# Kernel optimization log

Measured on AMD Instinct MI355X. Metric: run time of the kernel, lower is better.

Reference implementation:

```python
import jax, jax.numpy as jnp
import numpy as np

N = 50000
E = 800000
D_IN = 384
D_H = 128
D_MLP = 128
K = 16


def layer_norm(x, g, b, eps=1e-5):
    m = x.mean(-1, keepdims=True)
    v = ((x - m) ** 2).mean(-1, keepdims=True)
    return (x - m) / jnp.sqrt(v + eps) * g + b


def setup_inputs() -> dict:
    key = jax.random.key(0)
    ks = jax.random.split(key, 16)
    s = lambda d: 1.0 / np.sqrt(d)
    return {
        "x": jax.random.normal(ks[0], (N, D_IN), jnp.float32),
        "edge_index": jax.random.randint(ks[1], (2, E), 0, N, jnp.int64),
        # GCNConv 1
        "W1": jax.random.normal(ks[2], (D_IN, D_H), jnp.float32) * s(D_IN),
        "b1": jnp.zeros((D_H,), jnp.float32),
        "g1": jnp.ones((D_H,), jnp.float32),
        "be1": jnp.zeros((D_H,), jnp.float32),
        # GCNConv 2
        "W2": jax.random.normal(ks[3], (D_H, D_H), jnp.float32) * s(D_H),
        "b2": jnp.zeros((D_H,), jnp.float32),
        "g2": jnp.ones((D_H,), jnp.float32),
        "be2": jnp.zeros((D_H,), jnp.float32),
        # residual projection (input_dim != conv_hidden)
        "rW": jax.random.normal(ks[4], (D_IN, D_H), jnp.float32) * s(D_IN),
        "rb": jnp.zeros((D_H,), jnp.float32),
        "rg": jnp.ones((D_H,), jnp.float32),
        "rbe": jnp.zeros((D_H,), jnp.float32),
        # MLP head
        "mW1": jax.random.normal(ks[5], (D_H, D_MLP), jnp.float32) * s(D_H),
        "mb1": jnp.zeros((D_MLP,), jnp.float32),
        "mg": jnp.ones((D_MLP,), jnp.float32),
        "mbe": jnp.zeros((D_MLP,), jnp.float32),
        "mW2": jax.random.normal(ks[6], (D_MLP, K), jnp.float32) * s(D_MLP),
        "mb2": jnp.zeros((K,), jnp.float32),
    }


def reference(x, edge_index, W1, b1, g1, be1, W2, b2, g2, be2,
              rW, rb, rg, rbe, mW1, mb1, mg, mbe, mW2, mb2):
    n = x.shape[0]
    loops = jnp.arange(n, dtype=edge_index.dtype)
    src = jnp.concatenate([edge_index[0], loops])  # [E+N]
    dst = jnp.concatenate([edge_index[1], loops])
    # symmetric GCN normalization with self-loops
    deg = jax.ops.segment_sum(jnp.ones_like(src, x.dtype), dst, num_segments=n)
    dinv = jnp.where(deg > 0, jax.lax.rsqrt(deg), 0.0)
    norm = dinv[src] * dinv[dst]  # [E+N]

    def gcn_conv(h, W, b):
        hw = h @ W  # [N, D_H]
        msg = hw[src] * norm[:, None]  # gather + scale, [E+N, D_H]
        return jax.ops.segment_sum(msg, dst, num_segments=n) + b

    # layer 1 with projected residual
    h = jax.nn.elu(layer_norm(gcn_conv(x, W1, b1), g1, be1))
    h = h + layer_norm(x @ rW + rb, rg, rbe)
    # layer 2 with identity residual
    h = jax.nn.elu(layer_norm(gcn_conv(h, W2, b2), g2, be2)) + h
    # MLP head (dropout inactive in eval) + softmax over clusters
    z = jax.nn.elu(layer_norm(h @ mW1 + mb1, mg, mbe))
    H = z @ mW2 + mb2
    return jax.nn.softmax(H, axis=1)
```

## Files before the change

### kernel.cpp

```cpp
#include <hip/hip_runtime.h>

#define DH 128

typedef __attribute__((ext_vector_type(8))) short short8;
typedef __attribute__((ext_vector_type(4))) float f32x4;

__device__ __forceinline__ float wave_sum(float v) {
    #pragma unroll
    for (int o = 32; o > 0; o >>= 1) v += __shfl_xor(v, o, 64);
    return v;
}

__device__ __forceinline__ void ln_pair(float v0, float v1, float& o0, float& o1) {
    float m = wave_sum(v0 + v1) * (1.f / 128.f);
    float d0 = v0 - m, d1 = v1 - m;
    float var = wave_sum(d0 * d0 + d1 * d1) * (1.f / 128.f);
    float inv = rsqrtf(var + 1e-5f);
    o0 = d0 * inv; o1 = d1 * inv;
}

__device__ __forceinline__ float elu(float x) { return x > 0.f ? x : expm1f(x); }

__device__ __forceinline__ unsigned short f2bf(float f) {
    unsigned u = __float_as_uint(f);
    u += 0x7fffu + ((u >> 16) & 1u);
    return (unsigned short)(u >> 16);
}
__device__ __forceinline__ float bfl(unsigned u) { return __uint_as_float(u << 16); }
__device__ __forceinline__ float bfh(unsigned u) { return __uint_as_float(u & 0xffff0000u); }
__device__ __forceinline__ unsigned pack_bf2(float a, float b) {
    return (unsigned)f2bf(a) | ((unsigned)f2bf(b) << 16);
}
__device__ __forceinline__ short8 cvt8(float4 v0, float4 v1) {
    short8 o;
    o[0] = (short)f2bf(v0.x); o[1] = (short)f2bf(v0.y);
    o[2] = (short)f2bf(v0.z); o[3] = (short)f2bf(v0.w);
    o[4] = (short)f2bf(v1.x); o[5] = (short)f2bf(v1.y);
    o[6] = (short)f2bf(v1.z); o[7] = (short)f2bf(v1.w);
    return o;
}

__device__ __forceinline__ int xcd_work(int bid, int nwg) {
    int qc = nwg >> 3, rc = nwg & 7;
    int xcd = bid & 7, ix = bid >> 3;
    return (xcd < rc ? xcd * (qc + 1) : rc * (qc + 1) + (xcd - rc) * qc) + ix;
}

__global__ void deg_count_k(const int* __restrict__ dst, int* __restrict__ deg, int E) {
    int e = blockIdx.x * 256 + threadIdx.x;
    if (e < E) atomicAdd(&deg[dst[e]], 1);
}

__global__ __launch_bounds__(1024) void scan_part_k(const int* __restrict__ deg,
                                                    int* __restrict__ rowptr,
                                                    int* __restrict__ bsum,
                                                    float* __restrict__ dinv, int n)
{
    __shared__ int wsum[16];
    const int tid = threadIdx.x, lane = tid & 63, wid = tid >> 6;
    int i = blockIdx.x * 1024 + tid;
    int v = (i < n) ? deg[i] : 0;
    if (i < n) dinv[i] = rsqrtf((float)(v + 1));
    int s = v;
    #pragma unroll
    for (int o = 1; o < 64; o <<= 1) {
        int t = __shfl_up(s, o, 64);
        if (lane >= o) s += t;
    }
    if (lane == 63) wsum[wid] = s;
    __syncthreads();
    if (tid < 16) {
        int ws = wsum[tid];
        #pragma unroll
        for (int o = 1; o < 16; o <<= 1) {
            int t = __shfl_up(ws, o, 64);
            if (tid >= o) ws += t;
        }
        wsum[tid] = ws;
    }
    __syncthreads();
    int excl = (wid ? wsum[wid - 1] : 0) + s - v;
    if (i < n) rowptr[i] = excl;
    if (tid == 0) bsum[blockIdx.x] = wsum[15];
}

__global__ void scan_top_k(int* __restrict__ bsum, int* __restrict__ rowptr_n, int nb) {
    int lane = threadIdx.x;
    int carry = 0;
    for (int base = 0; base < nb; base += 64) {
        int i = base + lane;
        int v = (i < nb) ? bsum[i] : 0;
        int s = v;
        #pragma unroll
        for (int o = 1; o < 64; o <<= 1) {
            int t = __shfl_up(s, o, 64);
            if (lane >= o) s += t;
        }
        if (i < nb) bsum[i] = carry + s - v;
        carry += __shfl(s, 63, 64);
    }
    if (lane == 0) *rowptr_n = carry;
}

__global__ void scan_add_k(const int* __restrict__ bsum, int* __restrict__ rowptr,
                           int* __restrict__ cursor, int n)
{
    int i = blockIdx.x * 256 + threadIdx.x;
    if (i < n) {
        int v = rowptr[i] + bsum[i >> 10];
        rowptr[i] = v;
        cursor[i] = v;
    }
}

__global__ void fill_k(const int* __restrict__ src, const int* __restrict__ dst,
                       const float* __restrict__ dinv, int* __restrict__ cursor,
                       int2* __restrict__ csr, int E)
{
    int e = blockIdx.x * 256 + threadIdx.x;
    if (e < E) {
        int s = src[e], d = dst[e];
        float w = dinv[s] * dinv[d];
        int p = atomicAdd(&cursor[d], 1);
        csr[p] = make_int2(s, __float_as_int(w));
    }
}

__global__ void repack_zero_k(const float* __restrict__ W1, const float* __restrict__ rW,
                              const float* __restrict__ W2, const float* __restrict__ mW1,
                              unsigned short* __restrict__ Wp, int* __restrict__ deg, int n)
{
    int idx = blockIdx.x * 256 + threadIdx.x;
    if (idx < n) deg[idx] = 0;
    if (idx >= 131072) return;
    const float* W; int base;
    if (idx < 49152)       { W = W1;  base = 0; }
    else if (idx < 98304)  { W = rW;  base = 49152; }
    else if (idx < 114688) { W = W2;  base = 98304; }
    else                   { W = mW1; base = 114688; }
    int l = idx - base;
    int kb = l >> 12, rem = l & 4095;
    int nn = rem >> 5, ki = rem & 31;
    Wp[idx] = f2bf(W[(kb * 32 + ki) * DH + nn]);
}

__global__ __launch_bounds__(256, 4) void gemm1_k(
    const float* __restrict__ Af,
    const unsigned short* __restrict__ Bp1, const unsigned short* __restrict__ Bp2,
    const float* __restrict__ bb,
    unsigned short* __restrict__ outa, unsigned short* __restrict__ outb, int n)
{
    constexpr int K = 384, NKB = 12;
    __shared__ __align__(16) unsigned short smem[12288];
    unsigned short* smB = smem + 8192;

    const int tid = threadIdx.x;
    const int wid = tid >> 6, lane = tid & 63;
    const int m16 = lane & 15, q = lane >> 4;

    const int work = xcd_work(blockIdx.x, gridDim.x);
    const int rblk = work >> 2;
    const int var  = work & 3;
    const int mat = var >> 1;
    const int c0  = (var & 1) * 64;
    const unsigned short* Bp = mat ? Bp2 : Bp1;
    unsigned short* outp = mat ? outb : outa;
    const float* bias = mat ? bb : nullptr;
    const long long rowbase = (long long)rblk * 128;

    const int row_s0 = tid >> 2, c16_0 = tid & 3;
    const int row_s1 = (tid + 256) >> 2;
    long long gr0 = rowbase + row_s0; if (gr0 > (long long)n - 1) gr0 = n - 1;
    long long gr1 = rowbase + row_s1; if (gr1 > (long long)n - 1) gr1 = n - 1;
    const float* pA0 = Af + gr0 * K + c16_0 * 8;
    const float* pA1 = Af + gr1 * K + c16_0 * 8;
    unsigned short* dA0 = smem + row_s0 * 32 + ((c16_0 ^ (row_s0 & 3)) * 8);
    unsigned short* dA1 = smem + row_s1 * 32 + ((c16_0 ^ (row_s1 & 3)) * 8);
    const unsigned short* pB = Bp + c0 * 32 + tid * 8;
    unsigned short* dB = smB + (tid & 3) * 512 + (tid >> 2) * 8;

    float4 raf[2][2][2];
    short8 rbv[2];

    auto loadT = [&](int kb, int buf) {
        raf[buf][0][0] = *(const float4*)(pA0 + kb * 32);
        raf[buf][0][1] = *(const float4*)(pA0 + kb * 32 + 4);
        raf[buf][1][0] = *(const float4*)(pA1 + kb * 32);
        raf[buf][1][1] = *(const float4*)(pA1 + kb * 32 + 4);
        rbv[buf] = *(const short8*)(pB + kb * 4096);
    };
    auto writeT = [&](int buf) {
        *(short8*)(dA0 + buf * 4096) = cvt8(raf[buf][0][0], raf[buf][0][1]);
        *(short8*)(dA1 + buf * 4096) = cvt8(raf[buf][1][0], raf[buf][1][1]);
        *(short8*)(dB + buf * 2048) = rbv[buf];
    };

    f32x4 acc[2][4];
    const f32x4 zero = {0.f, 0.f, 0.f, 0.f};
    #pragma unroll
    for (int mi = 0; mi < 2; ++mi)
        #pragma unroll
        for (int nj = 0; nj < 4; ++nj) acc[mi][nj] = zero;

    const int frow = wid * 32 + m16;
    const unsigned short* fa_base = smem + frow * 32 + ((q ^ (m16 & 3)) * 8);
    const unsigned short* fb_base = smB + q * 512 + m16 * 8;

    loadT(0, 0);
    loadT(1, 1);
    writeT(0);
    __syncthreads();

    #pragma unroll
    for (int kb = 0; kb < NKB; ++kb) {
        const int buf = kb & 1;
        short8 af0 = *(const short8*)(fa_base + buf * 4096);
        short8 af1 = *(const short8*)(fa_base + buf * 4096 + 512);
        short8 bf[4];
        #pragma unroll
        for (int nj = 0; nj < 4; ++nj)
            bf[nj] = *(const short8*)(fb_base + buf * 2048 + nj * 128);
        if (kb + 2 < NKB) loadT(kb + 2, kb & 1);
        if (kb + 1 < NKB) writeT((kb + 1) & 1);
        #pragma unroll
        for (int nj = 0; nj < 4; ++nj) {
            acc[0][nj] = __builtin_amdgcn_mfma_f32_16x16x32_bf16(af0, bf[nj], acc[0][nj], 0, 0, 0);
            acc[1][nj] = __builtin_amdgcn_mfma_f32_16x16x32_bf16(af1, bf[nj], acc[1][nj], 0, 0, 0);
        }
        __syncthreads();
    }

    #pragma unroll
    for (int nj = 0; nj < 4; ++nj) {
        int cl = nj * 16 + m16;
        float bv = bias ? bias[c0 + cl] : 0.f;
        #pragma unroll
        for (int mi = 0; mi < 2; ++mi)
            #pragma unroll
            for (int r = 0; r < 4; ++r)
                smem[(wid * 32 + mi * 16 + q * 4 + r) * 72 + cl] = f2bf(acc[mi][nj][r] + bv);
    }
    __syncthreads();
    #pragma unroll
    for (int h = 0; h < 4; ++h) {
        int idx = tid + h * 256;
        int row = idx >> 3, c8 = idx & 7;
        long long grow = rowbase + row;
        if (grow < n)
            *(short8*)(outp + grow * DH + c0 + c8 * 8) = *(const short8*)(smem + row * 72 + c8 * 8);
    }
}

__global__ __launch_bounds__(256, 3) void gemm_k128(
    const unsigned short* __restrict__ A,
    const unsigned short* __restrict__ Bp, const float* __restrict__ bias,
    unsigned short* __restrict__ outp, int n)
{
    __shared__ __align__(16) unsigned short smem[24576];
    unsigned short* smB = smem + 16384;

    const int tid = threadIdx.x;
    const int wid = tid >> 6, lane = tid & 63;
    const int m16 = lane & 15, q = lane >> 4;

    const int work = xcd_work(blockIdx.x, gridDim.x);
    const int rblk = work >> 1;
    const int c0 = (work & 1) * 64;
    const long long rowbase = (long long)rblk * 128;

    #pragma unroll
    for (int r = 0; r < 8; ++r) {
        int j = r * 256 + tid;
        int row = j >> 4, c16 = j & 15;
        long long grow = rowbase + row; if (grow > (long long)n - 1) grow = n - 1;
        *(short8*)(smem + row * 128 + ((c16 ^ (row & 15)) * 8)) =
            *(const short8*)(A + grow * 128 + c16 * 8);
    }
    #pragma unroll
    for (int r = 0; r < 4; ++r) {
        int j = r * 256 + tid;
        int kb = j >> 8, rem = j & 255;
        int cl = rem >> 2, qq = rem & 3;
        *(short8*)(smB + kb * 2048 + qq * 512 + cl * 8) =
            *(const short8*)(Bp + kb * 4096 + c0 * 32 + rem * 8);
    }
    __syncthreads();

    f32x4 acc[2][4];
    const f32x4 zero = {0.f, 0.f, 0.f, 0.f};
    #pragma unroll
    for (int mi = 0; mi < 2; ++mi)
        #pragma unroll
        for (int nj = 0; nj < 4; ++nj) acc[mi][nj] = zero;

    const int frow = wid * 32 + m16;
    #pragma unroll
    for (int kb = 0; kb < 4; ++kb) {
        short8 af0 = *(const short8*)(smem + frow * 128 + (((kb * 4 + q) ^ m16) * 8));
        short8 af1 = *(const short8*)(smem + (frow + 16) * 128 + (((kb * 4 + q) ^ m16) * 8));
        #pragma unroll
        for (int nj = 0; nj < 4; ++nj) {
            short8 bf = *(const short8*)(smB + kb * 2048 + q * 512 + (nj * 16 + m16) * 8);
            acc[0][nj] = __builtin_amdgcn_mfma_f32_16x16x32_bf16(af0, bf, acc[0][nj], 0, 0, 0);
            acc[1][nj] = __builtin_amdgcn_mfma_f32_16x16x32_bf16(af1, bf, acc[1][nj], 0, 0, 0);
        }
    }

    __syncthreads();
    #pragma unroll
    for (int nj = 0; nj < 4; ++nj) {
        int cl = nj * 16 + m16;
        float bv = bias ? bias[c0 + cl] : 0.f;
        #pragma unroll
        for (int mi = 0; mi < 2; ++mi)
            #pragma unroll
            for (int r = 0; r < 4; ++r)
                smem[(wid * 32 + mi * 16 + q * 4 + r) * 72 + cl] = f2bf(acc[mi][nj][r] + bv);
    }
    __syncthreads();
    #pragma unroll
    for (int h = 0; h < 4; ++h) {
        int idx = tid + h * 256;
        int row = idx >> 3, c8 = idx & 7;
        long long grow = rowbase + row;
        if (grow < n)
            *(short8*)(outp + grow * DH + c0 + c8 * 8) = *(const short8*)(smem + row * 72 + c8 * 8);
    }
}

__device__ __forceinline__ void gather_row(
    const unsigned* __restrict__ hw, const int2* __restrict__ csr,
    int beg, int end, int lane, float& o0, float& o1)
{
    float a0 = 0.f, a1 = 0.f, b0 = 0.f, b1 = 0.f;
    float c0 = 0.f, c1 = 0.f, d0 = 0.f, d1 = 0.f;
    int p = beg;
    for (; p + 7 < end; p += 8) {
        int2 e0 = csr[p],     e1 = csr[p + 1], e2 = csr[p + 2], e3 = csr[p + 3];
        int2 e4 = csr[p + 4], e5 = csr[p + 5], e6 = csr[p + 6], e7 = csr[p + 7];
        unsigned u0 = hw[(long long)e0.x * 64 + lane];
        unsigned u1 = hw[(long long)e1.x * 64 + lane];
        unsigned u2 = hw[(long long)e2.x * 64 + lane];
        unsigned u3 = hw[(long long)e3.x * 64 + lane];
        unsigned u4 = hw[(long long)e4.x * 64 + lane];
        unsigned u5 = hw[(long long)e5.x * 64 + lane];
        unsigned u6 = hw[(long long)e6.x * 64 + lane];
        unsigned u7 = hw[(long long)e7.x * 64 + lane];
        float w0 = __int_as_float(e0.y), w1 = __int_as_float(e1.y);
        float w2 = __int_as_float(e2.y), w3 = __int_as_float(e3.y);
        float w4 = __int_as_float(e4.y), w5 = __int_as_float(e5.y);
        float w6 = __int_as_float(e6.y), w7 = __int_as_float(e7.y);
        a0 = fmaf(w0, bfl(u0), a0);  a1 = fmaf(w0, bfh(u0), a1);
        b0 = fmaf(w1, bfl(u1), b0);  b1 = fmaf(w1, bfh(u1), b1);
        c0 = fmaf(w2, bfl(u2), c0);  c1 = fmaf(w2, bfh(u2), c1);
        d0 = fmaf(w3, bfl(u3), d0);  d1 = fmaf(w3, bfh(u3), d1);
        a0 = fmaf(w4, bfl(u4), a0);  a1 = fmaf(w4, bfh(u4), a1);
        b0 = fmaf(w5, bfl(u5), b0);  b1 = fmaf(w5, bfh(u5), b1);
        c0 = fmaf(w6, bfl(u6), c0);  c1 = fmaf(w6, bfh(u6), c1);
        d0 = fmaf(w7, bfl(u7), d0);  d1 = fmaf(w7, bfh(u7), d1);
    }
    for (; p + 3 < end; p += 4) {
        int2 e0 = csr[p], e1 = csr[p + 1], e2 = csr[p + 2], e3 = csr[p + 3];
        unsigned u0 = hw[(long long)e0.x * 64 + lane];
        unsigned u1 = hw[(long long)e1.x * 64 + lane];
        unsigned u2 = hw[(long long)e2.x * 64 + lane];
        unsigned u3 = hw[(long long)e3.x * 64 + lane];
        float w0 = __int_as_float(e0.y), w1 = __int_as_float(e1.y);
        float w2 = __int_as_float(e2.y), w3 = __int_as_float(e3.y);
        a0 = fmaf(w0, bfl(u0), a0);  a1 = fmaf(w0, bfh(u0), a1);
        b0 = fmaf(w1, bfl(u1), b0);  b1 = fmaf(w1, bfh(u1), b1);
        c0 = fmaf(w2, bfl(u2), c0);  c1 = fmaf(w2, bfh(u2), c1);
        d0 = fmaf(w3, bfl(u3), d0);  d1 = fmaf(w3, bfh(u3), d1);
    }
    for (; p < end; ++p) {
        int2 e0 = csr[p];
        unsigned u0 = hw[(long long)e0.x * 64 + lane];
        float w0 = __int_as_float(e0.y);
        a0 = fmaf(w0, bfl(u0), a0);
        a1 = fmaf(w0, bfh(u0), a1);
    }
    o0 = (a0 + b0) + (c0 + d0);
    o1 = (a1 + b1) + (c1 + d1);
}

__global__ __launch_bounds__(256) void gfuse1_k(
    const unsigned* __restrict__ hw, const unsigned* __restrict__ proj,
    const int* __restrict__ rowptr, const int2* __restrict__ csr,
    const float* __restrict__ dinv,
    const float* __restrict__ b1, const float* __restrict__ g1, const float* __restrict__ be1,
    const float* __restrict__ rg, const float* __restrict__ rbe,
    unsigned* __restrict__ hout, int n)
{
    int row = blockIdx.x * 4 + (threadIdx.x >> 6);
    if (row >= n) return;
    int lane = threadIdx.x & 63;
    float a0, a1;
    gather_row(hw, csr, rowptr[row], rowptr[row + 1], lane, a0, a1);
    long long off = (long long)row * 64;
    float di = dinv[row], sl = di * di;
    unsigned us = hw[off + lane];
    float2 bv  = *(const float2*)(b1 + 2 * lane);
    float2 gv  = *(const float2*)(g1 + 2 * lane);
    float2 bev = *(const float2*)(be1 + 2 * lane);
    float2 rgv = *(const float2*)(rg + 2 * lane);
    float2 rbv = *(const float2*)(rbe + 2 * lane);
    float v0 = a0 + sl * bfl(us) + bv.x;
    float v1 = a1 + sl * bfh(us) + bv.y;
    float o0, o1; ln_pair(v0, v1, o0, o1);
    float t0 = elu(o0 * gv.x + bev.x);
    float t1 = elu(o1 * gv.y + bev.y);
    unsigned up = proj[off + lane];
    float q0, q1; ln_pair(bfl(up), bfh(up), q0, q1);
    hout[off + lane] = pack_bf2(t0 + q0 * rgv.x + rbv.x, t1 + q1 * rgv.y + rbv.y);
}

__global__ __launch_bounds__(256) void gfuse2_k(
    const unsigned* __restrict__ hw, const unsigned* __restrict__ hprev,
    const int* __restrict__ rowptr, const int2* __restrict__ csr,
    const float* __restrict__ dinv,
    const float* __restrict__ b2, const float* __restrict__ g2, const float* __restrict__ be2,
    unsigned* __restrict__ h2, int n)
{
    int row = blockIdx.x * 4 + (threadIdx.x >> 6);
    if (row >= n) return;
    int lane = threadIdx.x & 63;
    float a0, a1;
    gather_row(hw, csr, rowptr[row], rowptr[row + 1], lane, a0, a1);
    long long off = (long long)row * 64;
    float di = dinv[row], sl = di * di;
    unsigned us = hw[off + lane];
    float2 bv  = *(const float2*)(b2 + 2 * lane);
    float2 gv  = *(const float2*)(g2 + 2 * lane);
    float2 bev = *(const float2*)(be2 + 2 * lane);
    float v0 = a0 + sl * bfl(us) + bv.x;
    float v1 = a1 + sl * bfh(us) + bv.y;
    float o0, o1; ln_pair(v0, v1, o0, o1);
    float t0 = elu(o0 * gv.x + bev.x);
    float t1 = elu(o1 * gv.y + bev.y);
    unsigned uh = hprev[off + lane];
    h2[off + lane] = pack_bf2(t0 + bfl(uh), t1 + bfh(uh));
}

__global__ __launch_bounds__(256) void head_k(
    const unsigned* __restrict__ zraw, const float* __restrict__ g, const float* __restrict__ be,
    const float* __restrict__ mW2, const float* __restrict__ mb2,
    float* __restrict__ out, int n)
{
    int row = blockIdx.x * 4 + (threadIdx.x >> 6);
    if (row >= n) return;
    int lane = threadIdx.x & 63;
    unsigned u = zraw[(long long)row * 64 + lane];
    float o0, o1; ln_pair(bfl(u), bfh(u), o0, o1);
    float2 gv  = *(const float2*)(g + 2 * lane);
    float2 bev = *(const float2*)(be + 2 * lane);
    float z0 = elu(o0 * gv.x + bev.x);
    float z1 = elu(o1 * gv.y + bev.y);
    int k = lane & 15, seg = lane >> 4;
    float acc = 0.f;
    #pragma unroll
    for (int t = 0; t < 16; ++t) {
        int srcl = seg * 16 + t;
        float zz0 = __shfl(z0, srcl, 64);
        float zz1 = __shfl(z1, srcl, 64);
        int c = seg * 32 + 2 * t;
        acc = fmaf(zz0, mW2[c * 16 + k], acc);
        acc = fmaf(zz1, mW2[(c + 1) * 16 + k], acc);
    }
    acc += __shfl_xor(acc, 32, 64);
    acc += __shfl_xor(acc, 16, 64);
    float hk = acc + mb2[k];
    float mx = hk;
    #pragma unroll
    for (int o = 8; o > 0; o >>= 1) mx = fmaxf(mx, __shfl_xor(mx, o, 64));
    float e = expf(hk - mx);
    float s = e;
    #pragma unroll
    for (int o = 8; o > 0; o >>= 1) s += __shfl_xor(s, o, 64);
    if (lane < 16) out[(long long)row * 16 + k] = e / s;
}

static inline size_t align16(size_t x) { return (x + 15) & ~(size_t)15; }

extern "C" void kernel_launch(void* const* d_in, const int* in_sizes, int n_in,
                              void* d_out, int out_size, void* d_ws, size_t ws_size,
                              hipStream_t stream)
{
    const float* x   = (const float*)d_in[0];
    const int*   ei  = (const int*)d_in[1];
    const float* W1  = (const float*)d_in[2];
    const float* b1  = (const float*)d_in[3];
    const float* g1  = (const float*)d_in[4];
    const float* be1 = (const float*)d_in[5];
    const float* W2  = (const float*)d_in[6];
    const float* b2  = (const float*)d_in[7];
    const float* g2  = (const float*)d_in[8];
    const float* be2 = (const float*)d_in[9];
    const float* rW  = (const float*)d_in[10];
    const float* rb  = (const float*)d_in[11];
    const float* rg  = (const float*)d_in[12];
    const float* rbe = (const float*)d_in[13];
    const float* mW1 = (const float*)d_in[14];
    const float* mb1 = (const float*)d_in[15];
    const float* mg  = (const float*)d_in[16];
    const float* mbe = (const float*)d_in[17];
    const float* mW2 = (const float*)d_in[18];
    const float* mb2 = (const float*)d_in[19];
    float* out = (float*)d_out;

    const int n = in_sizes[0] / 384;
    const int E = in_sizes[1] / 2;
    const int* src = ei;
    const int* dst = ei + E;

    char* w = (char*)d_ws;
    int* deg     = (int*)w;   w += align16((size_t)n * 4);
    int* rowptr  = (int*)w;   w += align16((size_t)(n + 1) * 4);
    int* cursor  = (int*)w;   w += align16((size_t)n * 4);
    float* dinv  = (float*)w; w += align16((size_t)n * 4);
    int* bsum    = (int*)w;   w += align16((size_t)1024 * 4);
    int2* csr    = (int2*)w;  w += align16((size_t)E * 8);
    unsigned short* hw1  = (unsigned short*)w; w += align16((size_t)n * DH * 2);
    unsigned short* proj = (unsigned short*)w; w += align16((size_t)n * DH * 2);
    unsigned short* hbuf = (unsigned short*)w; w += align16((size_t)n * DH * 2);
    unsigned short* Wp   = (unsigned short*)w; w += align16((size_t)131072 * 2);
    unsigned short* Wp1 = Wp;
    unsigned short* Wpr = Wp + 49152;
    unsigned short* Wp2 = Wp + 98304;
    unsigned short* WpM = Wp + 114688;
    unsigned short* hw2  = hw1;
    unsigned short* h2   = proj;
    unsigned short* zraw = hbuf;

    int gE = (E + 255) / 256;
    int gN = (n + 255) / 256;
    int nb = (n + 1023) / 1024;
    int rblks = (n + 127) / 128;
    int gRow4 = (n + 3) / 4;

    repack_zero_k<<<512, 256, 0, stream>>>(W1, rW, W2, mW1, Wp, deg, n);

    deg_count_k<<<gE, 256, 0, stream>>>(dst, deg, E);
    scan_part_k<<<nb, 1024, 0, stream>>>(deg, rowptr, bsum, dinv, n);
    scan_top_k<<<1, 64, 0, stream>>>(bsum, rowptr + n, nb);
    scan_add_k<<<gN, 256, 0, stream>>>(bsum, rowptr, cursor, n);
    fill_k<<<gE, 256, 0, stream>>>(src, dst, dinv, cursor, csr, E);

    gemm1_k<<<rblks * 4, 256, 0, stream>>>(x, Wp1, Wpr, rb, hw1, proj, n);
    gfuse1_k<<<gRow4, 256, 0, stream>>>((unsigned*)hw1, (unsigned*)proj, rowptr, csr, dinv,
                                        b1, g1, be1, rg, rbe, (unsigned*)hbuf, n);

    gemm_k128<<<rblks * 2, 256, 0, stream>>>(hbuf, Wp2, nullptr, hw2, n);
    gfuse2_k<<<gRow4, 256, 0, stream>>>((unsigned*)hw2, (unsigned*)hbuf, rowptr, csr, dinv,
                                        b2, g2, be2, (unsigned*)h2, n);

    gemm_k128<<<rblks * 2, 256, 0, stream>>>(h2, WpM, mb1, zraw, n);
    head_k<<<gRow4, 256, 0, stream>>>((unsigned*)zraw, mg, mbe, mW2, mb2, out, n);
}
```

Baseline: 408.6 us.

## Partition CSR fill by XCD destination range and deepen gather unrolling

The CSR fill kernel now assigns each of 8 block groups (blockIdx & 7, matching round-robin XCD dispatch) a contiguous range of destination nodes. Each group scans all edges and only processes those whose destination falls in its range, so cursor atomics and CSR writes for a given node stay within one XCD's L2. The cost is that every group rereads the full dst array. Separately, the gather loop is unrolled to 16 outstanding row loads per iteration, with readfirstlane on the bounds, to raise memory-level parallelism at the cost of more registers.

```diff
diff --git a/kernel.cpp b/kernel.cpp
--- a/kernel.cpp
+++ b/kernel.cpp
@@ -113,16 +113,25 @@
     }
 }
 
-__global__ void fill_k(const int* __restrict__ src, const int* __restrict__ dst,
-                       const float* __restrict__ dinv, int* __restrict__ cursor,
-                       int2* __restrict__ csr, int E)
-{
-    int e = blockIdx.x * 256 + threadIdx.x;
-    if (e < E) {
-        int s = src[e], d = dst[e];
-        float w = dinv[s] * dinv[d];
-        int p = atomicAdd(&cursor[d], 1);
-        csr[p] = make_int2(s, __float_as_int(w));
+__global__ __launch_bounds__(256) void fill_xcd_k(
+    const int* __restrict__ src, const int* __restrict__ dst,
+    const float* __restrict__ dinv, int* __restrict__ cursor,
+    int2* __restrict__ csr, int E, int n)
+{
+    const int g   = blockIdx.x & 7;
+    const int j   = blockIdx.x >> 3;
+    const int bpg = gridDim.x >> 3;
+    const int per = (n + 7) >> 3;
+    const int lo = g * per;
+    const int hi = min(n, lo + per);
+    for (int e = j * 256 + threadIdx.x; e < E; e += bpg * 256) {
+        int d = dst[e];
+        if (d >= lo && d < hi) {
+            int s = src[e];
+            float w = dinv[s] * dinv[d];
+            int p = atomicAdd(&cursor[d], 1);
+            csr[p] = make_int2(s, __float_as_int(w));
+        }
     }
 }
 
@@ -332,32 +341,27 @@
     const unsigned* __restrict__ hw, const int2* __restrict__ csr,
     int beg, int end, int lane, float& o0, float& o1)
 {
+    beg = __builtin_amdgcn_readfirstlane(beg);
+    end = __builtin_amdgcn_readfirstlane(end);
     float a0 = 0.f, a1 = 0.f, b0 = 0.f, b1 = 0.f;
     float c0 = 0.f, c1 = 0.f, d0 = 0.f, d1 = 0.f;
     int p = beg;
-    for (; p + 7 < end; p += 8) {
-        int2 e0 = csr[p],     e1 = csr[p + 1], e2 = csr[p + 2], e3 = csr[p + 3];
-        int2 e4 = csr[p + 4], e5 = csr[p + 5], e6 = csr[p + 6], e7 = csr[p + 7];
-        unsigned u0 = hw[(long long)e0.x * 64 + lane];
-        unsigned u1 = hw[(long long)e1.x * 64 + lane];
-        unsigned u2 = hw[(long long)e2.x * 64 + lane];
-        unsigned u3 = hw[(long long)e3.x * 64 + lane];
-        unsigned u4 = hw[(long long)e4.x * 64 + lane];
-        unsigned u5 = hw[(long long)e5.x * 64 + lane];
-        unsigned u6 = hw[(long long)e6.x * 64 + lane];
-        unsigned u7 = hw[(long long)e7.x * 64 + lane];
-        float w0 = __int_as_float(e0.y), w1 = __int_as_float(e1.y);
-        float w2 = __int_as_float(e2.y), w3 = __int_as_float(e3.y);
-        float w4 = __int_as_float(e4.y), w5 = __int_as_float(e5.y);
-        float w6 = __int_as_float(e6.y), w7 = __int_as_float(e7.y);
-        a0 = fmaf(w0, bfl(u0), a0);  a1 = fmaf(w0, bfh(u0), a1);
-        b0 = fmaf(w1, bfl(u1), b0);  b1 = fmaf(w1, bfh(u1), b1);
-        c0 = fmaf(w2, bfl(u2), c0);  c1 = fmaf(w2, bfh(u2), c1);
-        d0 = fmaf(w3, bfl(u3), d0);  d1 = fmaf(w3, bfh(u3), d1);
-        a0 = fmaf(w4, bfl(u4), a0);  a1 = fmaf(w4, bfh(u4), a1);
-        b0 = fmaf(w5, bfl(u5), b0);  b1 = fmaf(w5, bfh(u5), b1);
-        c0 = fmaf(w6, bfl(u6), c0);  c1 = fmaf(w6, bfh(u6), c1);
-        d0 = fmaf(w7, bfl(u7), d0);  d1 = fmaf(w7, bfh(u7), d1);
+    for (; p + 15 < end; p += 16) {
+        int2 e[16];
+        #pragma unroll
+        for (int i = 0; i < 16; ++i) e[i] = csr[p + i];
+        unsigned u[16];
+        #pragma unroll
+        for (int i = 0; i < 16; ++i) u[i] = hw[(long long)e[i].x * 64 + lane];
+        #pragma unroll
+        for (int i = 0; i < 16; ++i) {
+            float w = __int_as_float(e[i].y);
+            float lo = bfl(u[i]), hi = bfh(u[i]);
+            if ((i & 3) == 0)      { a0 = fmaf(w, lo, a0); a1 = fmaf(w, hi, a1); }
+            else if ((i & 3) == 1) { b0 = fmaf(w, lo, b0); b1 = fmaf(w, hi, b1); }
+            else if ((i & 3) == 2) { c0 = fmaf(w, lo, c0); c1 = fmaf(w, hi, c1); }
+            else                   { d0 = fmaf(w, lo, d0); d1 = fmaf(w, hi, d1); }
+        }
     }
     for (; p + 3 < end; p += 4) {
         int2 e0 = csr[p], e1 = csr[p + 1], e2 = csr[p + 2], e3 = csr[p + 3];
@@ -543,7 +547,7 @@
     scan_part_k<<<nb, 1024, 0, stream>>>(deg, rowptr, bsum, dinv, n);
     scan_top_k<<<1, 64, 0, stream>>>(bsum, rowptr + n, nb);
     scan_add_k<<<gN, 256, 0, stream>>>(bsum, rowptr, cursor, n);
-    fill_k<<<gE, 256, 0, stream>>>(src, dst, dinv, cursor, csr, E);
+    fill_xcd_k<<<1024, 256, 0, stream>>>(src, dst, dinv, cursor, csr, E, n);
 
     gemm1_k<<<rblks * 4, 256, 0, stream>>>(x, Wp1, Wpr, rb, hw1, proj, n);
     gfuse1_k<<<gRow4, 256, 0, stream>>>((unsigned*)hw1, (unsigned*)proj, rowptr, csr, dinv,
```

Result: no change. 403.7 us (-1.2%).
